# Kernel optimization log

Measured on AMD Instinct MI355X. Metric: run time of the kernel, lower is better.

## Reference

```python
import jax, jax.numpy as jnp
import numpy as np

SHAPE = (4, 16, 16)          # (t, h, w) latent shape
E, H, L = 576, 16, 6         # embd_dim, n_head, n_layer
DK = E // H                  # head dim = 36
SEQ = int(np.prod(SHAPE))    # 1024
B = 2


def _layernorm(x, s, b):
    m = x.mean(-1, keepdims=True)
    v = ((x - m) ** 2).mean(-1, keepdims=True)
    return (x - m) * jax.lax.rsqrt(v + 1e-5) * s + b


def _masks():
    # causal lower-triangular mask and L1 distance-decay mask (FullAttention.__init__)
    causal = np.tril(np.ones((SEQ, SEQ), dtype=bool))
    grids = np.meshgrid(*[np.arange(s) for s in SHAPE], indexing='ij')
    coords = np.stack([g.ravel() for g in grids], -1)          # [SEQ, 3]
    dist = np.abs(coords[:, None, :] - coords[None, :, :]).sum(-1).astype(np.float32)
    dm = np.exp(-dist / dist[0, -1])                            # max distance = dist[0, SEQ-1]
    return jnp.asarray(causal), jnp.asarray(dm)


def setup_inputs() -> dict:
    key = jax.random.key(0)
    ks = jax.random.split(key, 12)
    f32 = jnp.float32
    std = 1.0 / np.sqrt(E)
    pe = E // 3
    d = {}
    d['x'] = jax.random.normal(ks[0], (B, *SHAPE, E), f32)
    d['sos'] = jax.random.normal(ks[1], (E,), f32) * 0.02
    d['pe0'] = jax.random.normal(ks[2], (SHAPE[0], pe), f32) * 0.01
    d['pe1'] = jax.random.normal(ks[3], (SHAPE[1], pe), f32) * 0.01
    d['pe2'] = jax.random.normal(ks[4], (SHAPE[2], pe), f32) * 0.01
    d['ln1_s'] = jnp.ones((L, E), f32); d['ln1_b'] = jnp.zeros((L, E), f32)
    d['wq'] = jax.random.normal(ks[5], (L, E, E), f32) * std
    d['wk'] = jax.random.normal(ks[6], (L, E, E), f32) * std
    d['wv'] = jax.random.normal(ks[7], (L, E, E), f32) * std
    d['wo'] = jax.random.normal(ks[8], (L, E, E), f32) * (1.0 / np.sqrt(E * L))
    d['bo'] = jnp.zeros((L, E), f32)
    d['ln2_s'] = jnp.ones((L, E), f32); d['ln2_b'] = jnp.zeros((L, E), f32)
    d['w1'] = jax.random.normal(ks[9], (L, E, 4 * E), f32) * std
    d['b1'] = jnp.zeros((L, 4 * E), f32)
    d['w2'] = jax.random.normal(ks[10], (L, 4 * E, E), f32) * (1.0 / np.sqrt(4 * E))
    d['b2'] = jnp.zeros((L, E), f32)
    return d


def _forward(x, sos, pe0, pe1, pe2, ln1_s, ln1_b, wq, wk, wv, wo, bo,
             ln2_s, ln2_b, w1, b1, w2, b2):
    b = x.shape[0]
    causal, dm = _masks()
    h = x.reshape(b, SEQ, E)
    # RightShift: prepend learned SOS token, drop last
    h = jnp.concatenate([jnp.broadcast_to(sos, (b, 1, E)), h[:, :-1]], axis=1)
    # AddBroadcastPosEmbed (dim=-1): per-axis embeddings concatenated on channels
    pos = jnp.concatenate([
        jnp.broadcast_to(pe0[:, None, None, :], (*SHAPE, E // 3)),
        jnp.broadcast_to(pe1[None, :, None, :], (*SHAPE, E // 3)),
        jnp.broadcast_to(pe2[None, None, :, :], (*SHAPE, E // 3)),
    ], axis=-1).reshape(SEQ, E)
    h = h + pos
    scale = 1.0 / np.sqrt(DK)
    for l in range(L):  # fixed small layer loop
        y = _layernorm(h, ln1_s[l], ln1_b[l])
        q = (y @ wq[l]).reshape(b, SEQ, H, DK).transpose(0, 2, 1, 3)
        k = (y @ wk[l]).reshape(b, SEQ, H, DK).transpose(0, 2, 1, 3)
        v = (y @ wv[l]).reshape(b, SEQ, H, DK).transpose(0, 2, 1, 3)
        s = jnp.einsum('bhqd,bhkd->bhqk', q, k) * scale
        s = s * dm                              # elementwise distance-decay mask
        s = jnp.where(causal, s, -jnp.inf)       # causal masked_fill
        a = jax.nn.softmax(s, axis=-1)
        o = jnp.einsum('bhqk,bhkd->bhqd', a, v)
        o = o.transpose(0, 2, 1, 3).reshape(b, SEQ, E) @ wo[l] + bo[l]
        h = h + o
        y = _layernorm(h, ln2_s[l], ln2_b[l])
        y1 = y @ w1[l] + b1[l]
        y1 = jax.nn.sigmoid(1.702 * y1) * y1     # GeLU2
        h = h + (y1 @ w2[l] + b2[l])
    return h.reshape(b, *SHAPE, E)


def reference(x, sos, pe0, pe1, pe2, ln1_s, ln1_b, wq, wk, wv, wo, bo,
              ln2_s, ln2_b, w1, b1, w2, b2):
    return _forward(x, sos, pe0, pe1, pe2, ln1_s, ln1_b, wq, wk, wv, wo, bo,
                    ln2_s, ln2_b, w1, b1, w2, b2)
```

## Files before the change

### kernel.cpp

```cpp
#include <hip/hip_runtime.h>


#define E_    576
#define SEQ_  1024
#define B_    2
#define NH_   16
#define DK_   36
#define DKP_  64
#define NL_   6
#define FF_   2304
#define ROWS_ 2048

typedef unsigned short u16;
typedef unsigned int u32;
typedef float f32x4 __attribute__((ext_vector_type(4)));
typedef __bf16 bf16x8 __attribute__((ext_vector_type(8)));

#define MFMA16(a, b, c) __builtin_amdgcn_mfma_f32_16x16x32_bf16((a), (b), (c), 0, 0, 0)

__device__ __forceinline__ float bf2f(u16 u) {
    return __uint_as_float(((unsigned)u) << 16);
}
__device__ __forceinline__ u16 f2bf(float f) {
    unsigned u = __float_as_uint(f);
    u += 0x7fffu + ((u >> 16) & 1u);
    return (u16)(u >> 16);
}
__device__ __forceinline__ float load_in(const void* p, size_t i, int isf32) {
    return isf32 ? ((const float*)p)[i] : bf2f(((const u16*)p)[i]);
}
__device__ __forceinline__ u16 load_in_bf(const void* p, size_t i, int isf32) {
    return isf32 ? f2bf(((const float*)p)[i]) : ((const u16*)p)[i];
}
__device__ __forceinline__ bf16x8 ldg8(const u16* p) {
    uint4 u = *(const uint4*)p;
    bf16x8 r;
    __builtin_memcpy(&r, &u, 16);
    return r;
}
__device__ __forceinline__ void gload_lds16(const u16* g, u16* l) {
    __builtin_amdgcn_global_load_lds(
        (const __attribute__((address_space(1))) unsigned int*)g,
        (__attribute__((address_space(3))) unsigned int*)l, 16, 0, 0);
}

__global__ void detect_kernel(const u16* __restrict__ x, int* __restrict__ flag)
{
    __shared__ float red[4];
    int lane = threadIdx.x & 63, wave = threadIdx.x >> 6;
    float mx = 0.f;
    for (int i = threadIdx.x; i < 4096; i += 256) {
        float v = fabsf(bf2f(x[i]));
        if (v < 3e38f) mx = fmaxf(mx, v);
    }
    for (int off = 1; off < 64; off <<= 1) mx = fmaxf(mx, __shfl_xor(mx, off));
    if (lane == 0) red[wave] = mx;
    __syncthreads();
    if (threadIdx.x == 0) {
        float m = fmaxf(fmaxf(red[0], red[1]), fmaxf(red[2], red[3]));
        *flag = (m > 1e6f) ? 1 : 0;
    }
}

__global__ __launch_bounds__(256) void repack_kernel(
    const void* __restrict__ wq, const void* __restrict__ wk,
    const void* __restrict__ wv, const void* __restrict__ wo,
    const void* __restrict__ w1, const void* __restrict__ w2,
    u16* __restrict__ wT, const int* __restrict__ flagp)
{
    __shared__ u32 tile[64 * 33];
    int isf32 = *flagp;
    int idx = blockIdx.x, l = blockIdx.z;
    const void* src;
    u16* dst;
    size_t sbase;
    int R, C, cx, ry;
    if (idx < 324) {
        int t4 = idx / 81, rem = idx - t4 * 81;
        ry = rem / 9; cx = rem % 9; R = 576; C = 576;
        src = (t4 == 0) ? wq : (t4 == 1) ? wk : (t4 == 2) ? wv : wo;
        sbase = (size_t)l * 331776;
        dst = wT + (size_t)l * 3981312 + t4 * 331776;
    } else if (idx < 648) {
        int rem = idx - 324;
        ry = rem / 36; cx = rem % 36; R = 576; C = 2304;
        src = w1; sbase = (size_t)l * 1327104;
        dst = wT + (size_t)l * 3981312 + 1327104;
    } else {
        int rem = idx - 648;
        ry = rem / 9; cx = rem % 9; R = 2304; C = 576;
        src = w2; sbase = (size_t)l * 1327104;
        dst = wT + (size_t)l * 3981312 + 2654208;
    }
    int r0 = ry * 64, c0 = cx * 64;
    int t = threadIdx.x;
    int chunk = t & 15, row = t >> 4;
    #pragma unroll
    for (int i = 0; i < 4; i++) {
        int rr = row + i * 16;
        size_t g = sbase + (size_t)(r0 + rr) * C + c0 + chunk * 4;
        u32 lo, hi;
        if (isf32) {
            f32x4 v = *(const f32x4*)((const float*)src + g);
            lo = (u32)f2bf(v[0]) | ((u32)f2bf(v[1]) << 16);
            hi = (u32)f2bf(v[2]) | ((u32)f2bf(v[3]) << 16);
        } else {
            uint2 v = *(const uint2*)((const u16*)src + g);
            lo = v.x; hi = v.y;
        }
        tile[rr * 33 + chunk * 2] = lo;
        tile[rr * 33 + chunk * 2 + 1] = hi;
    }
    __syncthreads();
    int p = t & 31, nl = t >> 5;
    #pragma unroll
    for (int i = 0; i < 8; i++) {
        int nn = nl + i * 8;
        u32 wA = tile[(2 * p) * 33 + (nn >> 1)];
        u32 wB = tile[(2 * p + 1) * 33 + (nn >> 1)];
        u32 a = (nn & 1) ? (wA >> 16) : (wA & 0xffffu);
        u32 b = (nn & 1) ? (wB >> 16) : (wB & 0xffffu);
        u32* d32 = (u32*)(dst + (size_t)(c0 + nn) * R + r0);
        d32[p] = a | (b << 16);
    }
}

__global__ void embed_kernel(
    const void* __restrict__ x, const void* __restrict__ sos,
    const void* __restrict__ pe0, const void* __restrict__ pe1,
    const void* __restrict__ pe2, float* __restrict__ h,
    const int* __restrict__ flagp)
{
    int isf32 = *flagp;
    int row = blockIdx.x;
    int e = threadIdx.x;
    int s = row & 1023;
    float v = (s == 0) ? load_in(sos, e, isf32)
                       : load_in(x, (size_t)(row - 1) * E_ + e, isf32);
    int t = s >> 8, hh = (s >> 4) & 15, ww = s & 15;
    float p = (e < 192) ? load_in(pe0, t * 192 + e, isf32)
            : (e < 384) ? load_in(pe1, hh * 192 + e - 192, isf32)
                        : load_in(pe2, ww * 192 + e - 384, isf32);
    h[(size_t)row * E_ + e] = v + p;
}

__global__ __launch_bounds__(256) void ln_kernel(
    const float* __restrict__ h, u16* __restrict__ y,
    const void* __restrict__ sc, const void* __restrict__ bi,
    int off0, const int* __restrict__ flagp)
{
    int isf32 = *flagp;
    int lane = threadIdx.x & 63, wave = threadIdx.x >> 6;
    int row = blockIdx.x * 4 + wave;
    const float* hr = h + (size_t)row * E_;
    float v[9], s = 0.f, sq = 0.f;
    for (int j = 0; j < 9; j++) {
        v[j] = hr[lane + j * 64];
        s += v[j];
        sq += v[j] * v[j];
    }
    for (int off = 1; off < 64; off <<= 1) {
        s += __shfl_xor(s, off);
        sq += __shfl_xor(sq, off);
    }
    float mean = s * (1.0f / E_);
    float var = sq * (1.0f / E_) - mean * mean;
    float r = rsqrtf(var + 1e-5f);
    for (int j = 0; j < 9; j++) {
        int e = lane + j * 64;
        float sce = load_in(sc, off0 + e, isf32);
        float bie = load_in(bi, off0 + e, isf32);
        y[(size_t)row * E_ + e] = f2bf((v[j] - mean) * r * sce + bie);
    }
}

template <int MODE, int SPLITK>
__global__ __launch_bounds__(256) void gemm_kernel(
    const u16* __restrict__ A, const u16* __restrict__ BtBase, int K,
    const void* __restrict__ bias, int boff, float* __restrict__ hbuf,
    u16* __restrict__ out, u16* __restrict__ qb, u16* __restrict__ kb,
    u16* __restrict__ vtb, const int* __restrict__ flagp)
{
    __shared__ u16 lA[8192];
    __shared__ u16 lB[4096];
    int t = threadIdx.x;
    int lane = t & 63, wave = t >> 6;
    int lw = lane & 15, lq = lane >> 4;
    int wx = wave >> 1, wy = wave & 1;
    int m0 = blockIdx.x * 128, n0 = blockIdx.y * 64;
    int z = blockIdx.z / SPLITK, kz = blockIdx.z % SPLITK;
    int Ks = K / SPLITK, kbase = kz * Ks;

    const u16* Bt = BtBase + (MODE == 0 ? (size_t)z * 331776 : 0);
    int rowS = t >> 3;
    int gc = (t & 7) ^ (rowS & 7);
    const u16* gA = A + (size_t)(m0 + rowS) * K + kbase + gc * 8;
    const u16* gB = Bt + (size_t)(n0 + rowS) * K + kbase + gc * 8;
    size_t rstep = (size_t)32 * K;

    f32x4 acc[4][2];
    for (int mi = 0; mi < 4; mi++)
        for (int ni = 0; ni < 2; ni++)
            for (int r = 0; r < 4; r++) acc[mi][ni][r] = 0.f;

    for (int kc = 0; kc < Ks; kc += 64) {
        #pragma unroll
        for (int ra = 0; ra < 4; ra++)
            gload_lds16(gA + ra * rstep + kc, &lA[ra * 2048 + t * 8]);
        #pragma unroll
        for (int rb = 0; rb < 2; rb++)
            gload_lds16(gB + rb * rstep + kc, &lB[rb * 2048 + t * 8]);
        __syncthreads();
        #pragma unroll
        for (int ks = 0; ks < 2; ks++) {
            int csw = ((ks * 4 + lq) ^ (lw & 7)) * 8;
            bf16x8 bf0 = ldg8(&lB[(wy * 32 + lw) * 64 + csw]);
            bf16x8 bf1 = ldg8(&lB[(wy * 32 + 16 + lw) * 64 + csw]);
            #pragma unroll
            for (int mi = 0; mi < 4; mi++) {
                bf16x8 af = ldg8(&lA[(wx * 64 + mi * 16 + lw) * 64 + csw]);
                acc[mi][0] = MFMA16(af, bf0, acc[mi][0]);
                acc[mi][1] = MFMA16(af, bf1, acc[mi][1]);
            }
        }
        __syncthreads();
    }

    int isf32 = (MODE != 0) ? *flagp : 0;
    #pragma unroll
    for (int ni = 0; ni < 2; ni++) {
        int n = n0 + wy * 32 + ni * 16 + lw;
        float bn = 0.f;
        if (MODE == 2 || ((MODE == 1 || MODE == 3) && kz == 0))
            bn = load_in(bias, boff + n, isf32);
        #pragma unroll
        for (int mi = 0; mi < 4; mi++) {
            #pragma unroll
            for (int r = 0; r < 4; r++) {
                int m = m0 + wx * 64 + mi * 16 + lq * 4 + r;
                float v = acc[mi][ni][r];
                if (MODE == 0) {
                    int b = m >> 10, s = m & 1023;
                    int head = n / 36, d = n - head * 36;
                    size_t bh = (size_t)(b * NH_ + head);
                    if (z == 0)
                        qb[(bh * SEQ_ + s) * DKP_ + d] = f2bf(v * (1.0f / 6.0f));
                    else if (z == 1)
                        kb[(bh * SEQ_ + s) * DKP_ + d] = f2bf(v);
                    else
                        vtb[(bh * DKP_ + d) * SEQ_ + s] = f2bf(v);
                } else if (MODE == 2) {
                    float tt = v + bn;
                    out[(size_t)m * FF_ + n] = f2bf(tt / (1.0f + __expf(-1.702f * tt)));
                } else {
                    atomicAdd(&hbuf[(size_t)m * E_ + n], v + bn);
                }
            }
        }
    }
}

__global__ __launch_bounds__(256) void attn_kernel(
    const u16* __restrict__ qb, const u16* __restrict__ kb,
    const u16* __restrict__ vtb, u16* __restrict__ ob)
{
    __shared__ u32 plds[4][16][33];
    __shared__ float sm[4][16], sl[4][16];
    __shared__ float so[4][16][52];
    int lane = threadIdx.x & 63, wave = threadIdx.x >> 6;
    int lw = lane & 15, lq = lane >> 4;
    int L = blockIdx.x;
    int bh = L & 31;
    int qt = 63 - (L >> 5);
    int head = bh & 15, b = bh >> 4;
    int q0 = qt * 16;

    const u16* qbase = qb + ((size_t)bh * SEQ_ + q0) * DKP_;
    bf16x8 qf0 = ldg8(qbase + lw * DKP_ + lq * 8);
    bf16x8 qf1 = ldg8(qbase + lw * DKP_ + 32 + lq * 8);

    int tq = q0 >> 8, hq = (q0 >> 4) & 15;
    float m_i[4], l_i[4], ew[4];
    f32x4 oacc[3];
    int qi[4];
    for (int r = 0; r < 4; r++) {
        m_i[r] = -1e30f;
        l_i[r] = 0.f;
        qi[r] = q0 + lq * 4 + r;
        ew[r] = __expf((float)abs(lw - (lq * 4 + r)) * (-1.0f / 33.0f));
    }
    for (int c = 0; c < 3; c++)
        for (int r = 0; r < 4; r++) oacc[c][r] = 0.f;

    int nch = (q0 + 79) >> 6;
    for (int c = wave; c < nch; c += 4) {
        int kv0 = c * 64;
        bool diag = (c == nch - 1);
        bf16x8 kf[4][2], vf[3][2];
        #pragma unroll
        for (int kvh = 0; kvh < 4; kvh++) {
            const u16* krow =
                kb + ((size_t)bh * SEQ_ + kv0 + kvh * 16 + lw) * DKP_ + lq * 8;
            kf[kvh][0] = ldg8(krow);
            kf[kvh][1] = ldg8(krow + 32);
        }
        #pragma unroll
        for (int c2 = 0; c2 < 3; c2++) {
            const u16* vrow =
                vtb + ((size_t)bh * DKP_ + c2 * 16 + lw) * SEQ_ + kv0 + lq * 8;
            vf[c2][0] = ldg8(vrow);
            vf[c2][1] = ldg8(vrow + 32);
        }
        f32x4 st[4];
        #pragma unroll
        for (int kvh = 0; kvh < 4; kvh++) {
            f32x4 tt;
            for (int r = 0; r < 4; r++) tt[r] = 0.f;
            tt = MFMA16(qf0, kf[kvh][0], tt);
            tt = MFMA16(qf1, kf[kvh][1], tt);
            st[kvh] = tt;
        }
        float sA[4];
        #pragma unroll
        for (int kvh = 0; kvh < 4; kvh++) {
            int kk = kv0 + kvh * 16;
            int d = abs((kk >> 8) - tq) + abs(((kk >> 4) & 15) - hq);
            sA[kvh] = __expf((float)d * (-1.0f / 33.0f));
        }
        #pragma unroll
        for (int r = 0; r < 4; r++) {
            float v0 = st[0][r] * (sA[0] * ew[r]);
            float v1 = st[1][r] * (sA[1] * ew[r]);
            float v2 = st[2][r] * (sA[2] * ew[r]);
            float v3 = st[3][r] * (sA[3] * ew[r]);
            if (diag) {
                if (kv0 + 0 * 16 + lw > qi[r]) v0 = -1e30f;
                if (kv0 + 1 * 16 + lw > qi[r]) v1 = -1e30f;
                if (kv0 + 2 * 16 + lw > qi[r]) v2 = -1e30f;
                if (kv0 + 3 * 16 + lw > qi[r]) v3 = -1e30f;
            }
            float m2 = fmaxf(fmaxf(v0, v1), fmaxf(v2, v3));
            for (int off = 1; off < 16; off <<= 1)
                m2 = fmaxf(m2, __shfl_xor(m2, off));
            float mn = fmaxf(m_i[r], m2);
            float alpha = __expf(m_i[r] - mn);
            m_i[r] = mn;
            float p0 = __expf(v0 - mn), p1 = __expf(v1 - mn);
            float p2 = __expf(v2 - mn), p3 = __expf(v3 - mn);
            u32 a01 = (u32)f2bf(p0) | ((u32)f2bf(p1) << 16);
            u32 a23 = (u32)f2bf(p2) | ((u32)f2bf(p3) << 16);
            u32 b01 = (u32)__shfl_xor((int)a01, 1);
            u32 b23 = (u32)__shfl_xor((int)a23, 1);
            if (!(lw & 1)) {
                int ro = lq * 4 + r, w2 = lw >> 1;
                plds[wave][ro][w2 + 0]  = ((b01 & 0xffffu) << 16) | (a01 & 0xffffu);
                plds[wave][ro][w2 + 8]  = (b01 & 0xffff0000u) | (a01 >> 16);
                plds[wave][ro][w2 + 16] = ((b23 & 0xffffu) << 16) | (a23 & 0xffffu);
                plds[wave][ro][w2 + 24] = (b23 & 0xffff0000u) | (a23 >> 16);
            }
            float rs = (p0 + p1) + (p2 + p3);
            for (int off = 1; off < 16; off <<= 1)
                rs += __shfl_xor(rs, off);
            l_i[r] = l_i[r] * alpha + rs;
            for (int c2 = 0; c2 < 3; c2++) oacc[c2][r] *= alpha;
        }
        __asm__ volatile("s_waitcnt lgkmcnt(0)" ::: "memory");
        uint4 u0 = *(const uint4*)&plds[wave][lw][lq * 4];
        uint4 u1 = *(const uint4*)&plds[wave][lw][16 + lq * 4];
        bf16x8 pf0, pf1;
        __builtin_memcpy(&pf0, &u0, 16);
        __builtin_memcpy(&pf1, &u1, 16);
        #pragma unroll
        for (int c2 = 0; c2 < 3; c2++) {
            oacc[c2] = MFMA16(pf0, vf[c2][0], oacc[c2]);
            oacc[c2] = MFMA16(pf1, vf[c2][1], oacc[c2]);
        }
    }
    #pragma unroll
    for (int r = 0; r < 4; r++) {
        int ro = lq * 4 + r;
        if (lw == 0) { sm[wave][ro] = m_i[r]; sl[wave][ro] = l_i[r]; }
        for (int c2 = 0; c2 < 3; c2++)
            so[wave][ro][c2 * 16 + lw] = oacc[c2][r];
    }
    __syncthreads();
    for (int i = threadIdx.x; i < 16 * DK_; i += 256) {
        int row = i / DK_, col = i - row * DK_;
        float M = fmaxf(fmaxf(sm[0][row], sm[1][row]),
                        fmaxf(sm[2][row], sm[3][row]));
        float Lm = 0.f, O = 0.f;
        #pragma unroll
        for (int w = 0; w < 4; w++) {
            float f = __expf(sm[w][row] - M);
            Lm += f * sl[w][row];
            O += f * so[w][row][col];
        }
        ob[((size_t)b * SEQ_ + q0 + row) * E_ + head * DK_ + col] = f2bf(O / Lm);
    }
}

__global__ void out_kernel(const float* __restrict__ h, void* __restrict__ out,
                           const int* __restrict__ flagp)
{
    int isf32 = *flagp;
    int i = blockIdx.x * blockDim.x + threadIdx.x;
    if (isf32) ((float*)out)[i] = h[i];
    else       ((u16*)out)[i] = f2bf(h[i]);
}

extern "C" void kernel_launch(void* const* d_in, const int* in_sizes, int n_in,
                              void* d_out, int out_size, void* d_ws,
                              size_t ws_size, hipStream_t stream)
{
    const void* x    = d_in[0];
    const void* sos  = d_in[1];
    const void* pe0  = d_in[2];
    const void* pe1  = d_in[3];
    const void* pe2  = d_in[4];
    const void* ln1s = d_in[5];
    const void* ln1b = d_in[6];
    const void* wq   = d_in[7];
    const void* wk   = d_in[8];
    const void* wv   = d_in[9];
    const void* wo   = d_in[10];
    const void* bo   = d_in[11];
    const void* ln2s = d_in[12];
    const void* ln2b = d_in[13];
    const void* w1   = d_in[14];
    const void* b1   = d_in[15];
    const void* w2   = d_in[16];
    const void* b2   = d_in[17];

    char* ws = (char*)d_ws;
    u16*   qbuf  = (u16*)(ws + 0);
    u16*   kbuf  = (u16*)(ws + 4194304);
    u16*   vtbuf = (u16*)(ws + 8388608);
    float* h     = (float*)(ws + 12582912);
    u16*   y     = (u16*)(ws + 17301504);
    u16*   o     = (u16*)(ws + 19660800);
    u16*   y1    = (u16*)(ws + 22020096);
    u16*   wT    = (u16*)(ws + 31457280);
    int*   flag  = (int*)(ws + 79233024);

    hipMemsetAsync(ws, 0, 12582912, stream);
    detect_kernel<<<1, 256, 0, stream>>>((const u16*)x, flag);
    repack_kernel<<<dim3(972, 1, 6), 256, 0, stream>>>(
        wq, wk, wv, wo, w1, w2, wT, flag);
    embed_kernel<<<ROWS_, E_, 0, stream>>>(x, sos, pe0, pe1, pe2, h, flag);

    for (int l = 0; l < NL_; l++) {
        u16* wTl = wT + (size_t)l * 3981312;
        ln_kernel<<<512, 256, 0, stream>>>(h, y, ln1s, ln1b, l * E_, flag);
        gemm_kernel<0, 1><<<dim3(16, 9, 3), 256, 0, stream>>>(
            y, wTl, E_, nullptr, 0, nullptr, nullptr, qbuf, kbuf, vtbuf, flag);
        attn_kernel<<<dim3(2048), 256, 0, stream>>>(qbuf, kbuf, vtbuf, o);
        gemm_kernel<1, 3><<<dim3(16, 9, 3), 256, 0, stream>>>(
            o, wTl + 995328, E_, bo, l * E_, h, nullptr, nullptr, nullptr, nullptr, flag);
        ln_kernel<<<512, 256, 0, stream>>>(h, y, ln2s, ln2b, l * E_, flag);
        gemm_kernel<2, 1><<<dim3(16, 36, 1), 256, 0, stream>>>(
            y, wTl + 1327104, E_, b1, l * FF_, nullptr, y1, nullptr, nullptr, nullptr, flag);
        gemm_kernel<3, 4><<<dim3(16, 9, 4), 256, 0, stream>>>(
            y1, wTl + 2654208, FF_, b2, l * E_, h, nullptr, nullptr, nullptr, nullptr, flag);
    }
    out_kernel<<<4608, 256, 0, stream>>>(h, d_out, flag);
}
```

Measured before the change: 872.7 us.

## Restructure attention so each wave owns a query tile with transposed MFMA scores

The attention kernel now assigns each wave its own 16-query tile, with a block covering 64 queries, instead of splitting the KV chunks of one 16-query tile across four waves. This removes the cross-wave LDS merge and the __syncthreads. The MFMA operands are swapped so scores come out transposed, with K rows permuted so the probabilities land directly in the B-operand layout. That eliminates the LDS round trip and shuffles for P and cuts the per-row shuffle reductions to two steps. The risks are a quarter as many blocks, each wave walking every KV chunk serially, and uneven work across waves due to causal triangle imbalance.

```diff
diff --git a/kernel.cpp b/kernel.cpp
--- a/kernel.cpp
+++ b/kernel.cpp
@@ -15,6 +15,7 @@
 typedef unsigned int u32;
 typedef float f32x4 __attribute__((ext_vector_type(4)));
 typedef __bf16 bf16x8 __attribute__((ext_vector_type(8)));
+typedef __bf16 bf16x4 __attribute__((ext_vector_type(4)));
 
 #define MFMA16(a, b, c) __builtin_amdgcn_mfma_f32_16x16x32_bf16((a), (b), (c), 0, 0, 0)
 
@@ -264,138 +265,140 @@
     const u16* __restrict__ qb, const u16* __restrict__ kb,
     const u16* __restrict__ vtb, u16* __restrict__ ob)
 {
-    __shared__ u32 plds[4][16][33];
-    __shared__ float sm[4][16], sl[4][16];
-    __shared__ float so[4][16][52];
     int lane = threadIdx.x & 63, wave = threadIdx.x >> 6;
     int lw = lane & 15, lq = lane >> 4;
     int L = blockIdx.x;
     int bh = L & 31;
-    int qt = 63 - (L >> 5);
+    int T = 15 - (L >> 5);
     int head = bh & 15, b = bh >> 4;
-    int q0 = qt * 16;
-
-    const u16* qbase = qb + ((size_t)bh * SEQ_ + q0) * DKP_;
-    bf16x8 qf0 = ldg8(qbase + lw * DKP_ + lq * 8);
-    bf16x8 qf1 = ldg8(qbase + lw * DKP_ + 32 + lq * 8);
-
-    int tq = q0 >> 8, hq = (q0 >> 4) & 15;
-    float m_i[4], l_i[4], ew[4];
+    int q0w = T * 64 + wave * 16;
+
+    const u16* qrow = qb + ((size_t)bh * SEQ_ + q0w + lw) * DKP_ + lq * 8;
+    bf16x8 qf0 = ldg8(qrow);
+    bf16x8 qf1 = ldg8(qrow + 32);
+
+    int tq = q0w >> 8, hq = (q0w >> 4) & 15;
+    int qg = q0w + lw;
+    int wq8 = (lq & 1) * 8;
+    float ew8[8];
+    #pragma unroll
+    for (int i = 0; i < 8; i++)
+        ew8[i] = __expf((float)abs(lw - (wq8 + i)) * (-1.0f / 33.0f));
+
+    float m_i = -1e30f, l_i = 0.f;
     f32x4 oacc[3];
-    int qi[4];
-    for (int r = 0; r < 4; r++) {
-        m_i[r] = -1e30f;
-        l_i[r] = 0.f;
-        qi[r] = q0 + lq * 4 + r;
-        ew[r] = __expf((float)abs(lw - (lq * 4 + r)) * (-1.0f / 33.0f));
-    }
-    for (int c = 0; c < 3; c++)
-        for (int r = 0; r < 4; r++) oacc[c][r] = 0.f;
-
-    int nch = (q0 + 79) >> 6;
-    for (int c = wave; c < nch; c += 4) {
+    #pragma unroll
+    for (int c2 = 0; c2 < 3; c2++)
+        #pragma unroll
+        for (int r = 0; r < 4; r++) oacc[c2][r] = 0.f;
+
+    int kperm = (lw >> 2) * 8 + (lw & 3);
+    const u16* kbh = kb + (size_t)bh * SEQ_ * DKP_;
+    const u16* vbh = vtb + (size_t)bh * DKP_ * SEQ_;
+
+    int nch = T + 1;
+    for (int c = 0; c < nch; c++) {
         int kv0 = c * 64;
-        bool diag = (c == nch - 1);
         bf16x8 kf[4][2], vf[3][2];
         #pragma unroll
         for (int kvh = 0; kvh < 4; kvh++) {
-            const u16* krow =
-                kb + ((size_t)bh * SEQ_ + kv0 + kvh * 16 + lw) * DKP_ + lq * 8;
-            kf[kvh][0] = ldg8(krow);
-            kf[kvh][1] = ldg8(krow + 32);
+            const u16* kp = kbh +
+                (size_t)(kv0 + (kvh >> 1) * 32 + (kvh & 1) * 4 + kperm) * DKP_
+                + lq * 8;
+            kf[kvh][0] = ldg8(kp);
+            kf[kvh][1] = ldg8(kp + 32);
         }
         #pragma unroll
         for (int c2 = 0; c2 < 3; c2++) {
-            const u16* vrow =
-                vtb + ((size_t)bh * DKP_ + c2 * 16 + lw) * SEQ_ + kv0 + lq * 8;
-            vf[c2][0] = ldg8(vrow);
-            vf[c2][1] = ldg8(vrow + 32);
+            const u16* vp = vbh + (size_t)(c2 * 16 + lw) * SEQ_ + kv0 + lq * 8;
+            vf[c2][0] = ldg8(vp);
+            vf[c2][1] = ldg8(vp + 32);
         }
         f32x4 st[4];
         #pragma unroll
         for (int kvh = 0; kvh < 4; kvh++) {
             f32x4 tt;
+            #pragma unroll
             for (int r = 0; r < 4; r++) tt[r] = 0.f;
-            tt = MFMA16(qf0, kf[kvh][0], tt);
-            tt = MFMA16(qf1, kf[kvh][1], tt);
+            tt = MFMA16(kf[kvh][0], qf0, tt);
+            tt = MFMA16(kf[kvh][1], qf1, tt);
             st[kvh] = tt;
         }
-        float sA[4];
+        int tk = kv0 >> 8, hk0 = (kv0 >> 4) & 15;
+        float sB[4];
+        #pragma unroll
+        for (int i = 0; i < 4; i++)
+            sB[i] = __expf((float)(abs(tq - tk) + abs(hq - hk0 - i))
+                           * (-1.0f / 33.0f));
+        float fh0 = sB[lq >> 1], fh1 = sB[(lq >> 1) + 2];
+        float vv[4][4];
         #pragma unroll
         for (int kvh = 0; kvh < 4; kvh++) {
-            int kk = kv0 + kvh * 16;
-            int d = abs((kk >> 8) - tq) + abs(((kk >> 4) & 15) - hq);
-            sA[kvh] = __expf((float)d * (-1.0f / 33.0f));
-        }
+            float fh = (kvh < 2) ? fh0 : fh1;
+            #pragma unroll
+            for (int r = 0; r < 4; r++)
+                vv[kvh][r] = st[kvh][r] * (fh * ew8[(kvh & 1) * 4 + r]);
+        }
+        if (c == nch - 1) {
+            #pragma unroll
+            for (int kvh = 0; kvh < 4; kvh++) {
+                int koff = kv0 + (kvh >> 1) * 32 + lq * 8 + (kvh & 1) * 4;
+                #pragma unroll
+                for (int r = 0; r < 4; r++)
+                    if (koff + r > qg) vv[kvh][r] = -1e30f;
+            }
+        }
+        float mloc =
+            fmaxf(fmaxf(fmaxf(fmaxf(vv[0][0], vv[0][1]), fmaxf(vv[0][2], vv[0][3])),
+                        fmaxf(fmaxf(vv[1][0], vv[1][1]), fmaxf(vv[1][2], vv[1][3]))),
+                  fmaxf(fmaxf(fmaxf(vv[2][0], vv[2][1]), fmaxf(vv[2][2], vv[2][3])),
+                        fmaxf(fmaxf(vv[3][0], vv[3][1]), fmaxf(vv[3][2], vv[3][3]))));
+        mloc = fmaxf(mloc, __shfl_xor(mloc, 16));
+        mloc = fmaxf(mloc, __shfl_xor(mloc, 32));
+        float mn = fmaxf(m_i, mloc);
+        float alpha = __expf(m_i - mn);
+        m_i = mn;
+        float p[4][4];
+        float rs = 0.f;
+        #pragma unroll
+        for (int kvh = 0; kvh < 4; kvh++) {
+            #pragma unroll
+            for (int r = 0; r < 4; r++) {
+                p[kvh][r] = __expf(vv[kvh][r] - mn);
+                rs += p[kvh][r];
+            }
+        }
+        rs += __shfl_xor(rs, 16);
+        rs += __shfl_xor(rs, 32);
+        l_i = l_i * alpha + rs;
+        #pragma unroll
+        for (int c2 = 0; c2 < 3; c2++)
+            #pragma unroll
+            for (int r = 0; r < 4; r++) oacc[c2][r] *= alpha;
+        bf16x8 pf0, pf1;
         #pragma unroll
         for (int r = 0; r < 4; r++) {
-            float v0 = st[0][r] * (sA[0] * ew[r]);
-            float v1 = st[1][r] * (sA[1] * ew[r]);
-            float v2 = st[2][r] * (sA[2] * ew[r]);
-            float v3 = st[3][r] * (sA[3] * ew[r]);
-            if (diag) {
-                if (kv0 + 0 * 16 + lw > qi[r]) v0 = -1e30f;
-                if (kv0 + 1 * 16 + lw > qi[r]) v1 = -1e30f;
-                if (kv0 + 2 * 16 + lw > qi[r]) v2 = -1e30f;
-                if (kv0 + 3 * 16 + lw > qi[r]) v3 = -1e30f;
-            }
-            float m2 = fmaxf(fmaxf(v0, v1), fmaxf(v2, v3));
-            for (int off = 1; off < 16; off <<= 1)
-                m2 = fmaxf(m2, __shfl_xor(m2, off));
-            float mn = fmaxf(m_i[r], m2);
-            float alpha = __expf(m_i[r] - mn);
-            m_i[r] = mn;
-            float p0 = __expf(v0 - mn), p1 = __expf(v1 - mn);
-            float p2 = __expf(v2 - mn), p3 = __expf(v3 - mn);
-            u32 a01 = (u32)f2bf(p0) | ((u32)f2bf(p1) << 16);
-            u32 a23 = (u32)f2bf(p2) | ((u32)f2bf(p3) << 16);
-            u32 b01 = (u32)__shfl_xor((int)a01, 1);
-            u32 b23 = (u32)__shfl_xor((int)a23, 1);
-            if (!(lw & 1)) {
-                int ro = lq * 4 + r, w2 = lw >> 1;
-                plds[wave][ro][w2 + 0]  = ((b01 & 0xffffu) << 16) | (a01 & 0xffffu);
-                plds[wave][ro][w2 + 8]  = (b01 & 0xffff0000u) | (a01 >> 16);
-                plds[wave][ro][w2 + 16] = ((b23 & 0xffffu) << 16) | (a23 & 0xffffu);
-                plds[wave][ro][w2 + 24] = (b23 & 0xffff0000u) | (a23 >> 16);
-            }
-            float rs = (p0 + p1) + (p2 + p3);
-            for (int off = 1; off < 16; off <<= 1)
-                rs += __shfl_xor(rs, off);
-            l_i[r] = l_i[r] * alpha + rs;
-            for (int c2 = 0; c2 < 3; c2++) oacc[c2][r] *= alpha;
-        }
-        __asm__ volatile("s_waitcnt lgkmcnt(0)" ::: "memory");
-        uint4 u0 = *(const uint4*)&plds[wave][lw][lq * 4];
-        uint4 u1 = *(const uint4*)&plds[wave][lw][16 + lq * 4];
-        bf16x8 pf0, pf1;
-        __builtin_memcpy(&pf0, &u0, 16);
-        __builtin_memcpy(&pf1, &u1, 16);
+            pf0[r]     = (__bf16)p[0][r];
+            pf0[4 + r] = (__bf16)p[1][r];
+            pf1[r]     = (__bf16)p[2][r];
+            pf1[4 + r] = (__bf16)p[3][r];
+        }
         #pragma unroll
         for (int c2 = 0; c2 < 3; c2++) {
-            oacc[c2] = MFMA16(pf0, vf[c2][0], oacc[c2]);
-            oacc[c2] = MFMA16(pf1, vf[c2][1], oacc[c2]);
-        }
-    }
-    #pragma unroll
-    for (int r = 0; r < 4; r++) {
-        int ro = lq * 4 + r;
-        if (lw == 0) { sm[wave][ro] = m_i[r]; sl[wave][ro] = l_i[r]; }
-        for (int c2 = 0; c2 < 3; c2++)
-            so[wave][ro][c2 * 16 + lw] = oacc[c2][r];
-    }
-    __syncthreads();
-    for (int i = threadIdx.x; i < 16 * DK_; i += 256) {
-        int row = i / DK_, col = i - row * DK_;
-        float M = fmaxf(fmaxf(sm[0][row], sm[1][row]),
-                        fmaxf(sm[2][row], sm[3][row]));
-        float Lm = 0.f, O = 0.f;
-        #pragma unroll
-        for (int w = 0; w < 4; w++) {
-            float f = __expf(sm[w][row] - M);
-            Lm += f * sl[w][row];
-            O += f * so[w][row][col];
-        }
-        ob[((size_t)b * SEQ_ + q0 + row) * E_ + head * DK_ + col] = f2bf(O / Lm);
+            oacc[c2] = MFMA16(vf[c2][0], pf0, oacc[c2]);
+            oacc[c2] = MFMA16(vf[c2][1], pf1, oacc[c2]);
+        }
+    }
+    float rl = 1.0f / l_i;
+    u16* obase = ob + ((size_t)b * SEQ_ + q0w + lw) * E_ + head * DK_;
+    #pragma unroll
+    for (int c2 = 0; c2 < 3; c2++) {
+        if (c2 < 2 || lq == 0) {
+            bf16x4 sv;
+            #pragma unroll
+            for (int r = 0; r < 4; r++) sv[r] = (__bf16)(oacc[c2][r] * rl);
+            *(bf16x4*)(obase + c2 * 16 + lq * 4) = sv;
+        }
     }
 }
 
@@ -453,7 +456,7 @@
         ln_kernel<<<512, 256, 0, stream>>>(h, y, ln1s, ln1b, l * E_, flag);
         gemm_kernel<0, 1><<<dim3(16, 9, 3), 256, 0, stream>>>(
             y, wTl, E_, nullptr, 0, nullptr, nullptr, qbuf, kbuf, vtbuf, flag);
-        attn_kernel<<<dim3(2048), 256, 0, stream>>>(qbuf, kbuf, vtbuf, o);
+        attn_kernel<<<dim3(512), 256, 0, stream>>>(qbuf, kbuf, vtbuf, o);
         gemm_kernel<1, 3><<<dim3(16, 9, 3), 256, 0, stream>>>(
             o, wTl + 995328, E_, bo, l * E_, h, nullptr, nullptr, nullptr, nullptr, flag);
         ln_kernel<<<512, 256, 0, stream>>>(h, y, ln2s, ln2b, l * E_, flag);
```

Result: slower. 894.7 us (+2.5%).
